# Performance work log

Measured on AMD Instinct MI355X. Metric: run time of the kernel, lower is better.

## Reference

```python
import jax, jax.numpy as jnp
import numpy as np

NUM_HEADS = 8
KEY_DIM = 64
WINDOW = 8
SHIFT = 4
B, H, W, C = 8, 64, 64, 512


def setup_inputs() -> dict:
    key = jax.random.key(0)
    ks = jax.random.split(key, 6)
    s = 0.02  # small init scale for numerically tame attention
    return {
        "x": jax.random.normal(ks[0], (B, H, W, C), jnp.float32),
        "wq": jax.random.normal(ks[1], (C, NUM_HEADS, KEY_DIM), jnp.float32) * s,
        "bq": jnp.zeros((NUM_HEADS, KEY_DIM), jnp.float32),
        "wk": jax.random.normal(ks[2], (C, NUM_HEADS, KEY_DIM), jnp.float32) * s,
        "bk": jnp.zeros((NUM_HEADS, KEY_DIM), jnp.float32),
        "wv": jax.random.normal(ks[3], (C, NUM_HEADS, KEY_DIM), jnp.float32) * s,
        "bv": jnp.zeros((NUM_HEADS, KEY_DIM), jnp.float32),
        "wo": jax.random.normal(ks[4], (NUM_HEADS, KEY_DIM, C), jnp.float32) * s,
        "bo": jnp.zeros((C,), jnp.float32),
    }


def reference(x, wq, bq, wk, bk, wv, bv, wo, bo):
    b, h, w, c = x.shape
    ws, ss = WINDOW, SHIFT
    pad_h = (ws - h % ws) % ws
    pad_w = (ws - w % ws) % ws
    padded = jnp.pad(x, ((0, 0), (0, pad_h), (0, pad_w), (0, 0)))
    if ss:
        padded = jnp.roll(padded, shift=(-ss, -ss), axis=(1, 2))
    ph, pw = h + pad_h, w + pad_w
    nh, nw = ph // ws, pw // ws
    # window partition: [B, nh, ws, nw, ws, C] -> [B*nh*nw, ws*ws, C]
    win = padded.reshape(b, nh, ws, nw, ws, c)
    win = win.transpose(0, 1, 3, 2, 4, 5).reshape(-1, ws * ws, c)
    q = jnp.einsum("ntc,chd->nthd", win, wq) + bq
    k = jnp.einsum("ntc,chd->nthd", win, wk) + bk
    v = jnp.einsum("ntc,chd->nthd", win, wv) + bv
    scale = 1.0 / jnp.sqrt(jnp.asarray(KEY_DIM, q.dtype))
    scores = jnp.einsum("nqhd,nkhd->nhqk", q, k) * scale
    attn = jax.nn.softmax(scores, axis=-1)
    out = jnp.einsum("nhqk,nkhd->nqhd", attn, v)
    proj = jnp.einsum("nqhd,hdc->nqc", out, wo) + bo
    # window merge
    merged = proj.reshape(b, nh, nw, ws, ws, c)
    merged = merged.transpose(0, 1, 3, 2, 4, 5).reshape(b, ph, pw, c)
    if ss:
        merged = jnp.roll(merged, shift=(ss, ss), axis=(1, 2))
    if pad_h or pad_w:
        merged = merged[:, :h, :w, :]
    return x + merged
```

## Files before the change

### kernel.cpp

```cpp
#include <hip/hip_runtime.h>

typedef unsigned short u16;
typedef short bf16x8 __attribute__((ext_vector_type(8)));
typedef float f32x4 __attribute__((ext_vector_type(4)));

typedef __attribute__((address_space(3))) unsigned int lds_uint;
typedef __attribute__((address_space(1))) const unsigned int glob_uint;

__device__ __forceinline__ void gll16(const void* g, void* l) {
    __builtin_amdgcn_global_load_lds((glob_uint*)g, (lds_uint*)l, 16, 0, 0);
}

__device__ __forceinline__ u16 f2b(float f) {
    union { float f; unsigned int u; } cv; cv.f = f;
    unsigned int u = cv.u;
    u += 0x7fffu + ((u >> 16) & 1u);
    return (u16)(u >> 16);
}

__device__ __forceinline__ uint2 pack4(float a, float b, float c, float d) {
    uint2 r;
    r.x = (unsigned int)f2b(a) | ((unsigned int)f2b(b) << 16);
    r.y = (unsigned int)f2b(c) | ((unsigned int)f2b(d) << 16);
    return r;
}

__global__ __launch_bounds__(256) void prep_pre_kernel(const float* __restrict__ x,
        const float* __restrict__ wq, const float* __restrict__ wk,
        const float* __restrict__ wv, const float* __restrict__ wo,
        const float* __restrict__ bq, const float* __restrict__ bk,
        const float* __restrict__ bv,
        u16* __restrict__ xw, u16* __restrict__ wqkvh, u16* __restrict__ woT,
        float* __restrict__ biash) {
    if (blockIdx.x < 8192) {
        int idx = blockIdx.x * 256 + threadIdx.x;
        int row = idx >> 6;
        int c = (idx & 63) * 8;
        int b_ = row >> 12, win = (row >> 6) & 63, t = row & 63;
        int wi = win >> 3, wj = win & 7, ti = t >> 3, tj = t & 7;
        int hh = (wi * 8 + ti + 4) & 63, ww = (wj * 8 + tj + 4) & 63;
        const float* src = x + ((size_t)b_ * 4096 + hh * 64 + ww) * 512 + c;
        float4 v0 = *(const float4*)src;
        float4 v1 = *(const float4*)(src + 4);
        ushort4 p0, p1;
        p0.x = f2b(v0.x); p0.y = f2b(v0.y); p0.z = f2b(v0.z); p0.w = f2b(v0.w);
        p1.x = f2b(v1.x); p1.y = f2b(v1.y); p1.z = f2b(v1.z); p1.w = f2b(v1.w);
        u16* dst = xw + (size_t)row * 512 + c;
        *(ushort4*)dst = p0;
        *(ushort4*)(dst + 4) = p1;
    } else {
        int idx = (blockIdx.x - 8192) * 256 + threadIdx.x;
        const int N1 = 512 * 1536;
        const int N2 = 512 * 512;
        if (idx < N1) {
            int k = idx / 1536, n2 = idx % 1536;
            int h = n2 / 192, j = n2 % 192;
            const float* w = (j < 64) ? wq : (j < 128) ? wk : wv;
            wqkvh[(size_t)n2 * 512 + k] = f2b(w[k * 512 + h * 64 + (j & 63)]);
        } else if (idx < N1 + N2) {
            int i = idx - N1;
            int k = i / 512, n = i % 512;
            woT[n * 512 + k] = f2b(wo[k * 512 + n]);
        } else if (idx < N1 + N2 + 1536) {
            int n2 = idx - N1 - N2;
            int h = n2 / 192, j = n2 % 192;
            const float* b = (j < 64) ? bq : (j < 128) ? bk : bv;
            biash[n2] = b[h * 64 + (j & 63)];
        }
    }
}

__global__ __launch_bounds__(512) void fused_qkv_attn(const u16* __restrict__ xw,
        const u16* __restrict__ wqkvh, const float* __restrict__ biash,
        u16* __restrict__ ows) {
    __shared__ u16 S[20480];
    const int tid = threadIdx.x;
    const int lane = tid & 63, wid = tid >> 6;
    const int wr = wid >> 1, wc = wid & 1;
    const int g = wid >> 2;
    const int slot = wid & 3;
    const int m = lane & 15, qd = lane >> 4;
    const int wp = blockIdx.x & 255;
    const int h = blockIdx.x >> 8;
    const int rowBase = wp * 128;

    u16* As  = S;
    u16* Bs  = S + 8192;
    u16* QKs = S;
    u16* VT  = S + 8704;
    u16* Pw  = S + 13312 + slot * 1152;

    const u16* Bsrc = wqkvh + (size_t)h * 192 * 512;
    f32x4 acc[2][6];
#pragma unroll
    for (int i = 0; i < 2; ++i)
#pragma unroll
        for (int j = 0; j < 6; ++j) acc[i][j] = (f32x4){0.f, 0.f, 0.f, 0.f};

    for (int kt = 0; kt < 8; ++kt) {
        const int k0 = kt * 64;
#pragma unroll
        for (int j = 0; j < 2; ++j) {
            int q = j * 512 + tid;
            int r = q >> 3, c = (q & 7) ^ (r & 7);
            gll16(xw + (size_t)(rowBase + r) * 512 + k0 + c * 8, As + q * 8);
        }
#pragma unroll
        for (int j = 0; j < 3; ++j) {
            int q = j * 512 + tid;
            int r = q >> 3, c = (q & 7) ^ (r & 7);
            gll16(Bsrc + (size_t)r * 512 + k0 + c * 8, Bs + q * 8);
        }
        __syncthreads();
#pragma unroll
        for (int s = 0; s < 2; ++s) {
            bf16x8 a[2], b[6];
#pragma unroll
            for (int ni = 0; ni < 6; ++ni) {
                int R = wc * 96 + ni * 16 + m;
                b[ni] = *(const bf16x8*)&Bs[R * 64 + (((s * 4 + qd) ^ (R & 7)) * 8)];
            }
#pragma unroll
            for (int mi = 0; mi < 2; ++mi) {
                int R = wr * 32 + mi * 16 + m;
                a[mi] = *(const bf16x8*)&As[R * 64 + (((s * 4 + qd) ^ (R & 7)) * 8)];
            }
#pragma unroll
            for (int mi = 0; mi < 2; ++mi)
#pragma unroll
                for (int ni = 0; ni < 6; ++ni)
                    acc[mi][ni] = __builtin_amdgcn_mfma_f32_16x16x32_bf16(b[ni], a[mi], acc[mi][ni], 0, 0, 0);
        }
        __syncthreads();
    }

    for (int w = 0; w < 2; ++w) {
        if (g == w) {
#pragma unroll
            for (int mi = 0; mi < 2; ++mi) {
                int t = (wr & 1) * 32 + mi * 16 + m;
#pragma unroll
                for (int ni = 0; ni < 6; ++ni) {
                    int cn = wc * 96 + ni * 16;
                    float4 bb = *(const float4*)&biash[h * 192 + cn + qd * 4];
                    if (cn < 128) {
                        *(uint2*)&QKs[t * 136 + cn + qd * 4] =
                            pack4(acc[mi][ni][0] + bb.x, acc[mi][ni][1] + bb.y,
                                  acc[mi][ni][2] + bb.z, acc[mi][ni][3] + bb.w);
                    } else {
                        int d0 = cn - 128 + qd * 4;
                        VT[(d0 + 0) * 72 + t] = f2b(acc[mi][ni][0] + bb.x);
                        VT[(d0 + 1) * 72 + t] = f2b(acc[mi][ni][1] + bb.y);
                        VT[(d0 + 2) * 72 + t] = f2b(acc[mi][ni][2] + bb.z);
                        VT[(d0 + 3) * 72 + t] = f2b(acc[mi][ni][3] + bb.w);
                    }
                }
            }
        }
        __syncthreads();

        if (g == w) {
            const int q0 = slot * 16;
            f32x4 sa[4];
#pragma unroll
            for (int ni = 0; ni < 4; ++ni) sa[ni] = (f32x4){0.f, 0.f, 0.f, 0.f};
#pragma unroll
            for (int s = 0; s < 2; ++s) {
                bf16x8 qf = *(const bf16x8*)&QKs[(q0 + m) * 136 + s * 32 + qd * 8];
#pragma unroll
                for (int ni = 0; ni < 4; ++ni) {
                    bf16x8 kf = *(const bf16x8*)&QKs[(ni * 16 + m) * 136 + 64 + s * 32 + qd * 8];
                    sa[ni] = __builtin_amdgcn_mfma_f32_16x16x32_bf16(qf, kf, sa[ni], 0, 0, 0);
                }
            }
            const float c1 = 0.125f * 1.4426950408889634f;
#pragma unroll
            for (int rr = 0; rr < 4; ++rr) {
                float mx = -3.4e38f;
#pragma unroll
                for (int ni = 0; ni < 4; ++ni) mx = fmaxf(mx, sa[ni][rr]);
                mx = fmaxf(mx, __shfl_xor(mx, 1, 64));
                mx = fmaxf(mx, __shfl_xor(mx, 2, 64));
                mx = fmaxf(mx, __shfl_xor(mx, 4, 64));
                mx = fmaxf(mx, __shfl_xor(mx, 8, 64));
                float sum = 0.f;
#pragma unroll
                for (int ni = 0; ni < 4; ++ni) {
                    float p = exp2f((sa[ni][rr] - mx) * c1);
                    sa[ni][rr] = p;
                    sum += p;
                }
                sum += __shfl_xor(sum, 1, 64);
                sum += __shfl_xor(sum, 2, 64);
                sum += __shfl_xor(sum, 4, 64);
                sum += __shfl_xor(sum, 8, 64);
                float inv = 1.f / sum;
                int r = qd * 4 + rr;
#pragma unroll
                for (int ni = 0; ni < 4; ++ni)
                    Pw[r * 72 + ni * 16 + m] = f2b(sa[ni][rr] * inv);
            }

            f32x4 oa[4];
#pragma unroll
            for (int ni = 0; ni < 4; ++ni) oa[ni] = (f32x4){0.f, 0.f, 0.f, 0.f};
#pragma unroll
            for (int s = 0; s < 2; ++s) {
                bf16x8 pf = *(const bf16x8*)&Pw[m * 72 + s * 32 + qd * 8];
#pragma unroll
                for (int ni = 0; ni < 4; ++ni) {
                    bf16x8 vf = *(const bf16x8*)&VT[(ni * 16 + m) * 72 + s * 32 + qd * 8];
                    oa[ni] = __builtin_amdgcn_mfma_f32_16x16x32_bf16(vf, pf, oa[ni], 0, 0, 0);
                }
            }
            {
                int win2 = wp * 2 + w;
                int t2 = q0 + m;
                int b_ = win2 >> 6, wh = (win2 >> 3) & 7, ww_ = win2 & 7;
                int ti = t2 >> 3, tj = t2 & 7;
                int hh = (wh * 8 + ti + 4) & 63;
                int www = (ww_ * 8 + tj + 4) & 63;
                size_t tok = (size_t)b_ * 4096 + hh * 64 + www;
                u16* dst = ows + tok * 512 + h * 64;
#pragma unroll
                for (int ni = 0; ni < 4; ++ni)
                    *(uint2*)&dst[ni * 16 + qd * 4] =
                        pack4(oa[ni][0], oa[ni][1], oa[ni][2], oa[ni][3]);
            }
        }
        __syncthreads();
    }
}

__global__ __launch_bounds__(256) void proj_gemm(const u16* __restrict__ ows,
        const u16* __restrict__ woT, const float* __restrict__ bo,
        const float* __restrict__ x, float* __restrict__ out) {
    __shared__ u16 S[16384];
    u16* As = S;
    u16* Bs = S + 8192;
    const int tid = threadIdx.x;
    const int lane = tid & 63, wid = tid >> 6;
    const int wr = wid >> 1, wc = wid & 1;
    const int m = lane & 15, qd = lane >> 4;
    const int rowBase = blockIdx.y * 128;
    const int colBase = blockIdx.x * 128;
    const int c8 = (lane & 7) ^ (lane >> 3);

    f32x4 acc[4][4];
#pragma unroll
    for (int i = 0; i < 4; ++i)
#pragma unroll
        for (int j = 0; j < 4; ++j) acc[i][j] = (f32x4){0.f, 0.f, 0.f, 0.f};

    for (int kt = 0; kt < 8; ++kt) {
        const int k0 = kt * 64;
        __syncthreads();
#pragma unroll
        for (int j = 0; j < 4; ++j) {
            int q = (j * 4 + wid) * 64 + lane;
            int r = (j * 4 + wid) * 8 + (lane >> 3);
            gll16(ows + (size_t)(rowBase + r) * 512 + k0 + c8 * 8, &As[q * 8]);
            gll16(woT + (size_t)(colBase + r) * 512 + k0 + c8 * 8, &Bs[q * 8]);
        }
        __syncthreads();
#pragma unroll
        for (int s = 0; s < 2; ++s) {
            bf16x8 a[4], b[4];
#pragma unroll
            for (int ni = 0; ni < 4; ++ni) {
                int R = wc * 64 + ni * 16 + m;
                b[ni] = *(const bf16x8*)&Bs[R * 64 + (((s * 4 + qd) ^ (R & 7)) * 8)];
            }
#pragma unroll
            for (int mi = 0; mi < 4; ++mi) {
                int R = wr * 64 + mi * 16 + m;
                a[mi] = *(const bf16x8*)&As[R * 64 + (((s * 4 + qd) ^ (R & 7)) * 8)];
            }
#pragma unroll
            for (int mi = 0; mi < 4; ++mi)
#pragma unroll
                for (int ni = 0; ni < 4; ++ni)
                    acc[mi][ni] = __builtin_amdgcn_mfma_f32_16x16x32_bf16(b[ni], a[mi], acc[mi][ni], 0, 0, 0);
        }
    }
    __syncthreads();

    float* Ct = (float*)S;
    for (int p = 0; p < 2; ++p) {
        if (wr == p) {
#pragma unroll
            for (int mi = 0; mi < 4; ++mi) {
                int r = mi * 16 + m;
#pragma unroll
                for (int ni = 0; ni < 4; ++ni) {
                    int ch = (wc * 16 + ni * 4 + qd) ^ (r & 7);
                    *(f32x4*)&Ct[r * 128 + ch * 4] = acc[mi][ni];
                }
            }
        }
        __syncthreads();
        {
            int k = tid >> 2, cseg = tid & 3;
            size_t tok = (size_t)(rowBase + p * 64 + k);
            const float* xs = &x[tok * 512 + colBase + cseg * 32];
            const float* bs = &bo[colBase + cseg * 32];
            float* os = &out[tok * 512 + colBase + cseg * 32];
#pragma unroll
            for (int j = 0; j < 8; ++j) {
                int ch = (cseg * 8 + j) ^ (k & 7);
                f32x4 c = *(const f32x4*)&Ct[k * 128 + ch * 4];
                float4 xv = *(const float4*)&xs[j * 4];
                float4 bv = *(const float4*)&bs[j * 4];
                float4 o;
                o.x = c[0] + bv.x + xv.x;
                o.y = c[1] + bv.y + xv.y;
                o.z = c[2] + bv.z + xv.z;
                o.w = c[3] + bv.w + xv.w;
                *(float4*)&os[j * 4] = o;
            }
        }
        __syncthreads();
    }
}

extern "C" void kernel_launch(void* const* d_in, const int* in_sizes, int n_in,
                              void* d_out, int out_size, void* d_ws, size_t ws_size,
                              hipStream_t stream) {
    const float* x  = (const float*)d_in[0];
    const float* wq = (const float*)d_in[1];
    const float* bq = (const float*)d_in[2];
    const float* wk = (const float*)d_in[3];
    const float* bk = (const float*)d_in[4];
    const float* wv = (const float*)d_in[5];
    const float* bv = (const float*)d_in[6];
    const float* wo = (const float*)d_in[7];
    const float* bo = (const float*)d_in[8];
    float* out = (float*)d_out;
    char* ws = (char*)d_ws;

    u16*   wqkvh = (u16*)ws;
    u16*   woT   = (u16*)(ws + 1572864);
    float* biash = (float*)(ws + 1572864 + 524288);
    size_t off = 2103296;
    u16* xw  = (u16*)(ws + off);
    u16* ows = xw + (size_t)16777216;

    const int prepN = 512 * 1536 + 512 * 512 + 1536;
    const int prepBlocks = (prepN + 255) / 256;
    prep_pre_kernel<<<dim3(8192 + prepBlocks), dim3(256), 0, stream>>>(
        x, wq, wk, wv, wo, bq, bk, bv, xw, wqkvh, woT, biash);
    fused_qkv_attn<<<dim3(2048), dim3(512), 0, stream>>>(xw, wqkvh, biash, ows);
    proj_gemm<<<dim3(4, 256), dim3(256), 0, stream>>>(ows, woT, bo, x, out);
}
```

Measured before the change: 256.3 us.

## Double-buffer QKV GEMM LDS tiles to overlap global loads with MFMA

Turns the QKV projection K-loop into a two-stage pipeline with ping-pong LDS buffers. Tile kt+1 is prefetched with global_load_lds while MFMAs run on tile kt, and a partial vmcnt wait covers only the older loads. This doubles the shared memory to 80KB per block, which may lower occupancy.

```diff
diff --git a/kernel.cpp b/kernel.cpp
--- a/kernel.cpp
+++ b/kernel.cpp
@@ -73,7 +73,7 @@
 __global__ __launch_bounds__(512) void fused_qkv_attn(const u16* __restrict__ xw,
         const u16* __restrict__ wqkvh, const float* __restrict__ biash,
         u16* __restrict__ ows) {
-    __shared__ u16 S[20480];
+    __shared__ u16 S[40960];
     const int tid = threadIdx.x;
     const int lane = tid & 63, wid = tid >> 6;
     const int wr = wid >> 1, wc = wid & 1;
@@ -84,8 +84,10 @@
     const int h = blockIdx.x >> 8;
     const int rowBase = wp * 128;
 
-    u16* As  = S;
-    u16* Bs  = S + 8192;
+    u16* const A0 = S;
+    u16* const B0 = S + 8192;
+    u16* const A1 = S + 20480;
+    u16* const B1 = S + 28672;
     u16* QKs = S;
     u16* VT  = S + 8704;
     u16* Pw  = S + 13312 + slot * 1152;
@@ -97,42 +99,67 @@
 #pragma unroll
         for (int j = 0; j < 6; ++j) acc[i][j] = (f32x4){0.f, 0.f, 0.f, 0.f};
 
-    for (int kt = 0; kt < 8; ++kt) {
-        const int k0 = kt * 64;
-#pragma unroll
-        for (int j = 0; j < 2; ++j) {
-            int q = j * 512 + tid;
-            int r = q >> 3, c = (q & 7) ^ (r & 7);
-            gll16(xw + (size_t)(rowBase + r) * 512 + k0 + c * 8, As + q * 8);
-        }
-#pragma unroll
-        for (int j = 0; j < 3; ++j) {
-            int q = j * 512 + tid;
-            int r = q >> 3, c = (q & 7) ^ (r & 7);
-            gll16(Bsrc + (size_t)r * 512 + k0 + c * 8, Bs + q * 8);
-        }
-        __syncthreads();
-#pragma unroll
-        for (int s = 0; s < 2; ++s) {
-            bf16x8 a[2], b[6];
-#pragma unroll
-            for (int ni = 0; ni < 6; ++ni) {
-                int R = wc * 96 + ni * 16 + m;
-                b[ni] = *(const bf16x8*)&Bs[R * 64 + (((s * 4 + qd) ^ (R & 7)) * 8)];
-            }
-#pragma unroll
-            for (int mi = 0; mi < 2; ++mi) {
-                int R = wr * 32 + mi * 16 + m;
-                a[mi] = *(const bf16x8*)&As[R * 64 + (((s * 4 + qd) ^ (R & 7)) * 8)];
-            }
-#pragma unroll
-            for (int mi = 0; mi < 2; ++mi)
-#pragma unroll
-                for (int ni = 0; ni < 6; ++ni)
-                    acc[mi][ni] = __builtin_amdgcn_mfma_f32_16x16x32_bf16(b[ni], a[mi], acc[mi][ni], 0, 0, 0);
-        }
-        __syncthreads();
-    }
+#define STAGE(K0, DA, DB)                                                    \
+    {                                                                        \
+        _Pragma("unroll")                                                    \
+        for (int j = 0; j < 2; ++j) {                                        \
+            int q = j * 512 + tid;                                           \
+            int r = q >> 3, c = (q & 7) ^ (r & 7);                           \
+            gll16(xw + (size_t)(rowBase + r) * 512 + (K0) + c * 8, (DA) + q * 8); \
+        }                                                                    \
+        _Pragma("unroll")                                                    \
+        for (int j = 0; j < 3; ++j) {                                        \
+            int q = j * 512 + tid;                                           \
+            int r = q >> 3, c = (q & 7) ^ (r & 7);                           \
+            gll16(Bsrc + (size_t)r * 512 + (K0) + c * 8, (DB) + q * 8);      \
+        }                                                                    \
+    }
+
+#define COMPUTE(SA, SB)                                                      \
+    _Pragma("unroll")                                                        \
+    for (int s = 0; s < 2; ++s) {                                            \
+        bf16x8 a[2], b[6];                                                   \
+        _Pragma("unroll")                                                    \
+        for (int ni = 0; ni < 6; ++ni) {                                     \
+            int R = wc * 96 + ni * 16 + m;                                   \
+            b[ni] = *(const bf16x8*)&(SB)[R * 64 + (((s * 4 + qd) ^ (R & 7)) * 8)]; \
+        }                                                                    \
+        _Pragma("unroll")                                                    \
+        for (int mi = 0; mi < 2; ++mi) {                                     \
+            int R = wr * 32 + mi * 16 + m;                                   \
+            a[mi] = *(const bf16x8*)&(SA)[R * 64 + (((s * 4 + qd) ^ (R & 7)) * 8)]; \
+        }                                                                    \
+        _Pragma("unroll")                                                    \
+        for (int mi = 0; mi < 2; ++mi)                                       \
+            _Pragma("unroll")                                                \
+            for (int ni = 0; ni < 6; ++ni)                                   \
+                acc[mi][ni] = __builtin_amdgcn_mfma_f32_16x16x32_bf16(       \
+                    b[ni], a[mi], acc[mi][ni], 0, 0, 0);                     \
+    }
+
+    {
+        u16 *cA = A0, *cB = B0, *nA = A1, *nB = B1;
+        STAGE(0, cA, cB);
+#pragma unroll 1
+        for (int kt = 0; kt < 7; ++kt) {
+            STAGE((kt + 1) * 64, nA, nB);
+            asm volatile("s_waitcnt vmcnt(5)" ::: "memory");
+            __builtin_amdgcn_s_barrier();
+            __builtin_amdgcn_sched_barrier(0);
+            COMPUTE(cA, cB);
+            __syncthreads();
+            u16* t;
+            t = cA; cA = nA; nA = t;
+            t = cB; cB = nB; nB = t;
+        }
+        asm volatile("s_waitcnt vmcnt(0)" ::: "memory");
+        __builtin_amdgcn_s_barrier();
+        __builtin_amdgcn_sched_barrier(0);
+        COMPUTE(cA, cB);
+        __syncthreads();
+    }
+#undef STAGE
+#undef COMPUTE
 
     for (int w = 0; w < 2; ++w) {
         if (g == w) {
```

Measured after the change: 291.7 us. +13.8%, slower.
